# Kernel optimization log

Hardware: AMD Instinct MI355X
Metric: run time of the kernel (lower is better)

## Reference

```python
import jax, jax.numpy as jnp
import numpy as np

B, L, D, H = 2, 2048, 2048, 16
HD = D // H  # 128

def setup_inputs() -> dict:
    key = jax.random.key(0)
    ks = jax.random.split(key, 12)
    s = 1.0 / np.sqrt(D)
    inp = {
        'x': jax.random.normal(ks[0], (B, L, D), jnp.float32),
        'sin': jax.random.normal(ks[1], (L, HD // 2), jnp.float32),
        'cos': jax.random.normal(ks[2], (L, HD // 2), jnp.float32),
        'mask': jnp.tril(jnp.ones((L, L), jnp.int32))[None, None],  # causal [1,1,L,L]
        'Wq': jax.random.normal(ks[3], (D, D), jnp.float32) * s,
        'bq': jnp.zeros((D,), jnp.float32),
        'Wk': jax.random.normal(ks[4], (D, D), jnp.float32) * s,
        'bk': jnp.zeros((D,), jnp.float32),
        'Wv': jax.random.normal(ks[5], (D, D), jnp.float32) * s,
        'bv': jnp.zeros((D,), jnp.float32),
        'Wo': jax.random.normal(ks[6], (D, D), jnp.float32) * s,
        'bo': jnp.zeros((D,), jnp.float32),
    }
    return inp

def reference(x, sin, cos, mask, Wq, bq, Wk, bk, Wv, bv, Wo, bo):
    Bx, Lx, Dx = x.shape
    q = (x @ Wq.T + bq).reshape(Bx, Lx, H, HD)
    k = (x @ Wk.T + bk).reshape(Bx, Lx, H, HD)
    v = (x @ Wv.T + bv).reshape(Bx, Lx, H, HD)
    half = HD // 2
    # partial rotary: note original computes q_rot*(cos - sin) (faithful)
    rot = (cos - sin)[:, None, :]  # [L,1,half]
    q = jnp.concatenate([q[..., :half] * rot, q[..., half:]], axis=-1)
    k = jnp.concatenate([k[..., :half] * rot, k[..., half:]], axis=-1)
    q = q.transpose(0, 2, 1, 3)  # [B,H,L,hd]
    k = k.transpose(0, 2, 1, 3)
    v = v.transpose(0, 2, 1, 3)
    scores = jnp.einsum('bhqd,bhkd->bhqk', q, k) / np.sqrt(HD).astype(np.float32)
    scores = jnp.where(mask == 0, -jnp.inf, scores)
    attn = jax.nn.softmax(scores, axis=-1)
    out = jnp.einsum('bhqk,bhkd->bhqd', attn, v)
    out = out.transpose(0, 2, 1, 3).reshape(Bx, Lx, Dx)
    return out @ Wo.T + bo
```

## Files before the change

kernel.cpp:

```cpp
#include <hip/hip_runtime.h>
#include <hip/hip_bf16.h>

typedef __attribute__((ext_vector_type(8))) short short8;
typedef __attribute__((ext_vector_type(4))) ushort ushort4v;
typedef __attribute__((ext_vector_type(4))) float f32x4;

#define MFMA16(A, B, C) __builtin_amdgcn_mfma_f32_16x16x32_bf16(A, B, C, 0, 0, 0)

#define GLOAD16(gp, lp)                                        \
  __builtin_amdgcn_global_load_lds(                            \
      (__attribute__((address_space(1))) void*)(gp),           \
      (__attribute__((address_space(3))) void*)(lp), 16, 0, 0)

static constexpr int Lx = 2048, Dx = 2048, Hx = 16, HDx = 128, NBx = 2;

__device__ __forceinline__ ushort f2bu(float f) {
  __hip_bfloat16 h = __float2bfloat16(f);
  union { __hip_bfloat16 h; ushort u; } v;
  v.h = h;
  return v.u;
}

__device__ __forceinline__ short8 pack8(const float4& a, const float4& b) {
  short8 r;
  r[0] = (short)f2bu(a.x); r[1] = (short)f2bu(a.y);
  r[2] = (short)f2bu(a.z); r[3] = (short)f2bu(a.w);
  r[4] = (short)f2bu(b.x); r[5] = (short)f2bu(b.y);
  r[6] = (short)f2bu(b.z); r[7] = (short)f2bu(b.w);
  return r;
}

__global__ void convert_kernel(const float* __restrict__ x,
                               const float* __restrict__ Wq,
                               const float* __restrict__ Wk,
                               const float* __restrict__ Wv,
                               const float* __restrict__ Wo,
                               ushort* __restrict__ xb, ushort* __restrict__ wqb,
                               ushort* __restrict__ wkb, ushort* __restrict__ wvb,
                               ushort* __restrict__ wob) {
  const int y = blockIdx.y;
  const float* s;
  ushort* d;
  int n;
  switch (y) {
    case 0: s = x;  d = xb;  n = NBx * Lx * Dx; break;
    case 1: s = Wq; d = wqb; n = Dx * Dx; break;
    case 2: s = Wk; d = wkb; n = Dx * Dx; break;
    case 3: s = Wv; d = wvb; n = Dx * Dx; break;
    default: s = Wo; d = wob; n = Dx * Dx; break;
  }
  const int stride = gridDim.x * blockDim.x * 8;
  for (int i = (blockIdx.x * blockDim.x + threadIdx.x) * 8; i < n; i += stride) {
    float4 a = *(const float4*)(s + i);
    float4 b = *(const float4*)(s + i + 4);
    *(short8*)(d + i) = pack8(a, b);
  }
}

__global__ __launch_bounds__(256, 2) void qkv_kernel(
    const ushort* __restrict__ xb,
    const ushort* __restrict__ wqb, const float* __restrict__ bq,
    const ushort* __restrict__ wkb, const float* __restrict__ bk,
    const ushort* __restrict__ wvb, const float* __restrict__ bv,
    const float* __restrict__ sinT, const float* __restrict__ cosT,
    ushort* __restrict__ qw, ushort* __restrict__ kw, ushort* __restrict__ vw) {
  const int z = blockIdx.z;
  const ushort* W   = (z == 0) ? wqb : (z == 1) ? wkb : wvb;
  const float* bias = (z == 0) ? bq : (z == 1) ? bk : bv;
  ushort* outp      = (z == 0) ? qw : (z == 1) ? kw : vw;

  const int bm = blockIdx.x, bn = blockIdx.y;
  const int tid = threadIdx.x;
  const int lane = tid & 63;
  const int w = tid >> 6;
  const int l15 = tid & 15, hi = (tid >> 4) & 3;
  const int wm = (w >> 1) * 64, wn = (w & 1) * 64;

  __shared__ ushort As[2][128 * 32];
  __shared__ ushort Bs[2][128 * 32];

  const int cA = w * 2;
  const int srow = cA * 16 + (lane >> 2);
  const int scol = (lane & 3) * 8;
  const ushort* aSrc = xb + (size_t)(bm * 128 + srow) * Dx + scol;
  const ushort* bSrc = W + (size_t)(bn * 128 + srow) * Dx + scol;
  const int ldsOff = cA * 512;

#define STAGE_QKV(buf, kt)                                           \
  do {                                                               \
    const ushort* ap = aSrc + (kt) * 32;                             \
    const ushort* bp = bSrc + (kt) * 32;                             \
    GLOAD16(ap, &As[buf][ldsOff]);                                   \
    GLOAD16(ap + 16 * Dx, &As[buf][ldsOff + 512]);                   \
    GLOAD16(bp, &Bs[buf][ldsOff]);                                   \
    GLOAD16(bp + 16 * Dx, &Bs[buf][ldsOff + 512]);                   \
  } while (0)

  f32x4 acc[4][4];
#pragma unroll
  for (int i = 0; i < 4; ++i)
#pragma unroll
    for (int j = 0; j < 4; ++j) acc[i][j] = {0.f, 0.f, 0.f, 0.f};

  STAGE_QKV(0, 0);
  __syncthreads();

  int cur = 0;
  for (int kt = 0; kt < 64; ++kt) {
    if (kt < 63) STAGE_QKV(cur ^ 1, kt + 1);
    short8 af[4], bf[4];
#pragma unroll
    for (int i = 0; i < 4; ++i)
      af[i] = *(const short8*)&As[cur][(wm + i * 16 + l15) * 32 + hi * 8];
#pragma unroll
    for (int j = 0; j < 4; ++j)
      bf[j] = *(const short8*)&Bs[cur][(wn + j * 16 + l15) * 32 + hi * 8];
#pragma unroll
    for (int i = 0; i < 4; ++i)
#pragma unroll
      for (int j = 0; j < 4; ++j) acc[i][j] = MFMA16(af[i], bf[j], acc[i][j]);
    __syncthreads();
    cur ^= 1;
  }
#undef STAGE_QKV

  const float rsHD = 0.08838834764831845f;
#pragma unroll
  for (int j = 0; j < 4; ++j) {
    const int n = bn * 128 + wn + j * 16 + l15;
    const int h = n >> 7, d = n & 127;
    const float bb = bias[n];
#pragma unroll
    for (int i = 0; i < 4; ++i) {
#pragma unroll
      for (int r = 0; r < 4; ++r) {
        const int m = bm * 128 + wm + i * 16 + hi * 4 + r;
        const int b = m >> 11, l = m & (Lx - 1);
        float v = acc[i][j][r] + bb;
        if (z < 2 && d < 64) v *= (cosT[l * 64 + d] - sinT[l * 64 + d]);
        if (z == 0) v *= rsHD;
        outp[(size_t)((b * Hx + h) * Lx + l) * HDx + d] = f2bu(v);
      }
    }
  }
}

__global__ __launch_bounds__(256, 2) void attn_kernel(
    const ushort* __restrict__ qw, const ushort* __restrict__ kw,
    const ushort* __restrict__ vw, ushort* __restrict__ ctx) {
  const int qt = (int)(gridDim.x - 1) - (int)blockIdx.x;
  const int bh = blockIdx.y;
  const int b = bh >> 4, h = bh & 15;
  const int tid = threadIdx.x;
  const int w = tid >> 6, l15 = tid & 15, hi = (tid >> 4) & 3;

  const ushort* Q = qw + (size_t)bh * Lx * HDx;
  const ushort* K = kw + (size_t)bh * Lx * HDx;
  const ushort* V = vw + (size_t)bh * Lx * HDx;

  __shared__ ushort Ks[64][136];
  __shared__ ushort Vt[128][72];
  __shared__ ushort Ps[4][16][72];

  short8 qf[4];
  {
    const ushort* qr = Q + (size_t)(qt * 64 + w * 16 + l15) * HDx + hi * 8;
#pragma unroll
    for (int ds = 0; ds < 4; ++ds) qf[ds] = *(const short8*)(qr + ds * 32);
  }

  f32x4 o[8];
#pragma unroll
  for (int df = 0; df < 8; ++df) o[df] = {0.f, 0.f, 0.f, 0.f};
  float mr[4], lr[4];
#pragma unroll
  for (int r = 0; r < 4; ++r) { mr[r] = -1e30f; lr[r] = 0.f; }

  const int skrow = tid >> 2, skd = (tid & 3) * 32;
  const int svk = (tid & 15) * 4, svd = (tid >> 4) * 8;

  for (int kv = 0; kv <= qt; ++kv) {
    __syncthreads();
    {
      const ushort* kp = K + (size_t)(kv * 64 + skrow) * HDx + skd;
      short8 k0 = *(const short8*)(kp + 0), k1 = *(const short8*)(kp + 8);
      short8 k2 = *(const short8*)(kp + 16), k3 = *(const short8*)(kp + 24);
      *(short8*)&Ks[skrow][skd + 0] = k0;
      *(short8*)&Ks[skrow][skd + 8] = k1;
      *(short8*)&Ks[skrow][skd + 16] = k2;
      *(short8*)&Ks[skrow][skd + 24] = k3;
    }
    {
      const ushort* vp = V + (size_t)(kv * 64 + svk) * HDx + svd;
      short8 r0 = *(const short8*)(vp);
      short8 r1 = *(const short8*)(vp + HDx);
      short8 r2 = *(const short8*)(vp + 2 * HDx);
      short8 r3 = *(const short8*)(vp + 3 * HDx);
#pragma unroll
      for (int j = 0; j < 8; ++j) {
        ushort4v pk;
        pk[0] = (ushort)r0[j]; pk[1] = (ushort)r1[j];
        pk[2] = (ushort)r2[j]; pk[3] = (ushort)r3[j];
        *(ushort4v*)&Vt[svd + j][svk] = pk;
      }
    }
    __syncthreads();

    f32x4 s[4];
#pragma unroll
    for (int kf = 0; kf < 4; ++kf) s[kf] = {0.f, 0.f, 0.f, 0.f};
#pragma unroll
    for (int kf = 0; kf < 4; ++kf)
#pragma unroll
      for (int ds = 0; ds < 4; ++ds) {
        short8 kb = *(const short8*)&Ks[kf * 16 + l15][ds * 32 + hi * 8];
        s[kf] = MFMA16(qf[ds], kb, s[kf]);
      }

    if (kv == qt) {
#pragma unroll
      for (int kf = 0; kf < 4; ++kf)
#pragma unroll
        for (int r = 0; r < 4; ++r)
          if (kf * 16 + l15 > w * 16 + hi * 4 + r) s[kf][r] = -1e30f;
    }

    float ml[4];
#pragma unroll
    for (int r = 0; r < 4; ++r)
      ml[r] = fmaxf(fmaxf(s[0][r], s[1][r]), fmaxf(s[2][r], s[3][r]));
#pragma unroll
    for (int off = 1; off <= 8; off <<= 1)
#pragma unroll
      for (int r = 0; r < 4; ++r) ml[r] = fmaxf(ml[r], __shfl_xor(ml[r], off));
    float scl[4];
#pragma unroll
    for (int r = 0; r < 4; ++r) {
      float mn = fmaxf(mr[r], ml[r]);
      scl[r] = __expf(mr[r] - mn);
      mr[r] = mn;
    }
    float ll[4] = {0.f, 0.f, 0.f, 0.f};
#pragma unroll
    for (int kf = 0; kf < 4; ++kf)
#pragma unroll
      for (int r = 0; r < 4; ++r) {
        float p = __expf(s[kf][r] - mr[r]);
        s[kf][r] = p;
        ll[r] += p;
      }
#pragma unroll
    for (int off = 1; off <= 8; off <<= 1)
#pragma unroll
      for (int r = 0; r < 4; ++r) ll[r] += __shfl_xor(ll[r], off);
#pragma unroll
    for (int r = 0; r < 4; ++r) lr[r] = lr[r] * scl[r] + ll[r];
#pragma unroll
    for (int df = 0; df < 8; ++df)
#pragma unroll
      for (int r = 0; r < 4; ++r) o[df][r] *= scl[r];

#pragma unroll
    for (int kf = 0; kf < 4; ++kf)
#pragma unroll
      for (int r = 0; r < 4; ++r)
        Ps[w][hi * 4 + r][kf * 16 + l15] = f2bu(s[kf][r]);

    short8 pa0 = *(const short8*)&Ps[w][l15][hi * 8];
    short8 pa1 = *(const short8*)&Ps[w][l15][32 + hi * 8];
#pragma unroll
    for (int df = 0; df < 8; ++df) {
      short8 v0 = *(const short8*)&Vt[df * 16 + l15][hi * 8];
      short8 v1 = *(const short8*)&Vt[df * 16 + l15][32 + hi * 8];
      o[df] = MFMA16(pa0, v0, o[df]);
      o[df] = MFMA16(pa1, v1, o[df]);
    }
  }

  float inv[4];
#pragma unroll
  for (int r = 0; r < 4; ++r) inv[r] = 1.0f / lr[r];
  ushort* cp = ctx + (size_t)(b * Lx + qt * 64 + w * 16) * Dx + h * HDx;
#pragma unroll
  for (int df = 0; df < 8; ++df)
#pragma unroll
    for (int r = 0; r < 4; ++r)
      cp[(size_t)(hi * 4 + r) * Dx + df * 16 + l15] = f2bu(o[df][r] * inv[r]);
}

__global__ __launch_bounds__(256, 2) void oproj_kernel(
    const ushort* __restrict__ ctx, const ushort* __restrict__ wob,
    const float* __restrict__ bo, float* __restrict__ out) {
  const int bm = blockIdx.x, bn = blockIdx.y;
  const int tid = threadIdx.x;
  const int lane = tid & 63;
  const int w = tid >> 6;
  const int l15 = tid & 15, hi = (tid >> 4) & 3;
  const int wm = (w >> 1) * 64, wn = (w & 1) * 64;

  __shared__ ushort As[2][128 * 32];
  __shared__ ushort Bs[2][128 * 32];

  const int cA = w * 2;
  const int srow = cA * 16 + (lane >> 2);
  const int scol = (lane & 3) * 8;
  const ushort* aSrc = ctx + (size_t)(bm * 128 + srow) * Dx + scol;
  const ushort* bSrc = wob + (size_t)(bn * 128 + srow) * Dx + scol;
  const int ldsOff = cA * 512;

#define STAGE_O(buf, kt)                                             \
  do {                                                               \
    const ushort* ap = aSrc + (kt) * 32;                             \
    const ushort* bp = bSrc + (kt) * 32;                             \
    GLOAD16(ap, &As[buf][ldsOff]);                                   \
    GLOAD16(ap + 16 * Dx, &As[buf][ldsOff + 512]);                   \
    GLOAD16(bp, &Bs[buf][ldsOff]);                                   \
    GLOAD16(bp + 16 * Dx, &Bs[buf][ldsOff + 512]);                   \
  } while (0)

  f32x4 acc[4][4];
#pragma unroll
  for (int i = 0; i < 4; ++i)
#pragma unroll
    for (int j = 0; j < 4; ++j) acc[i][j] = {0.f, 0.f, 0.f, 0.f};

  STAGE_O(0, 0);
  __syncthreads();

  int cur = 0;
  for (int kt = 0; kt < 64; ++kt) {
    if (kt < 63) STAGE_O(cur ^ 1, kt + 1);
    short8 af[4], bf[4];
#pragma unroll
    for (int i = 0; i < 4; ++i)
      af[i] = *(const short8*)&As[cur][(wm + i * 16 + l15) * 32 + hi * 8];
#pragma unroll
    for (int j = 0; j < 4; ++j)
      bf[j] = *(const short8*)&Bs[cur][(wn + j * 16 + l15) * 32 + hi * 8];
#pragma unroll
    for (int i = 0; i < 4; ++i)
#pragma unroll
      for (int j = 0; j < 4; ++j) acc[i][j] = MFMA16(af[i], bf[j], acc[i][j]);
    __syncthreads();
    cur ^= 1;
  }
#undef STAGE_O

#pragma unroll
  for (int j = 0; j < 4; ++j) {
    const int n = bn * 128 + wn + j * 16 + l15;
    const float bb = bo[n];
#pragma unroll
    for (int i = 0; i < 4; ++i)
#pragma unroll
      for (int r = 0; r < 4; ++r) {
        const int m = bm * 128 + wm + i * 16 + hi * 4 + r;
        out[(size_t)m * Dx + n] = acc[i][j][r] + bb;
      }
  }
}

extern "C" void kernel_launch(void* const* d_in, const int* in_sizes, int n_in,
                              void* d_out, int out_size, void* d_ws, size_t ws_size,
                              hipStream_t stream) {
  (void)in_sizes; (void)n_in; (void)out_size; (void)ws_size;
  const float* x    = (const float*)d_in[0];
  const float* sinT = (const float*)d_in[1];
  const float* cosT = (const float*)d_in[2];
  const float* Wq = (const float*)d_in[4];
  const float* bq = (const float*)d_in[5];
  const float* Wk = (const float*)d_in[6];
  const float* bk = (const float*)d_in[7];
  const float* Wv = (const float*)d_in[8];
  const float* bv = (const float*)d_in[9];
  const float* Wo = (const float*)d_in[10];
  const float* bo = (const float*)d_in[11];
  float* out = (float*)d_out;

  const size_t N = (size_t)NBx * Lx * Dx;
  const size_t M = (size_t)Dx * Dx;
  ushort* qw  = (ushort*)d_ws;
  ushort* kw  = qw + N;
  ushort* vw  = kw + N;
  ushort* ctx = vw + N;
  ushort* xb  = ctx;
  ushort* wqb = ctx + N;
  ushort* wkb = wqb + M;
  ushort* wvb = wkb + M;
  ushort* wob = wvb + M;

  convert_kernel<<<dim3(1024, 5), 256, 0, stream>>>(
      x, Wq, Wk, Wv, Wo, xb, wqb, wkb, wvb, wob);
  qkv_kernel<<<dim3(32, 16, 3), 256, 0, stream>>>(
      xb, wqb, bq, wkb, bk, wvb, bv, sinT, cosT, qw, kw, vw);
  attn_kernel<<<dim3(32, 32), 256, 0, stream>>>(qw, kw, vw, ctx);
  oproj_kernel<<<dim3(32, 16), 256, 0, stream>>>(ctx, wob, bo, out);
}
```

Baseline: 545.7 us.

## Pair causal query tiles per block and register-prefetch next K/V tile

Result: faster. 456.1 us (-16.4%).

```diff
diff --git a/kernel.cpp b/kernel.cpp
--- a/kernel.cpp
+++ b/kernel.cpp
@@ -148,7 +148,7 @@
 __global__ __launch_bounds__(256, 2) void attn_kernel(
     const ushort* __restrict__ qw, const ushort* __restrict__ kw,
     const ushort* __restrict__ vw, ushort* __restrict__ ctx) {
-  const int qt = (int)(gridDim.x - 1) - (int)blockIdx.x;
+  const int pair = blockIdx.x;
   const int bh = blockIdx.y;
   const int b = bh >> 4, h = bh & 15;
   const int tid = threadIdx.x;
@@ -159,133 +159,152 @@
   const ushort* V = vw + (size_t)bh * Lx * HDx;
 
   __shared__ ushort Ks[64][136];
-  __shared__ ushort Vt[128][72];
-  __shared__ ushort Ps[4][16][72];
-
-  short8 qf[4];
-  {
-    const ushort* qr = Q + (size_t)(qt * 64 + w * 16 + l15) * HDx + hi * 8;
-#pragma unroll
-    for (int ds = 0; ds < 4; ++ds) qf[ds] = *(const short8*)(qr + ds * 32);
-  }
-
-  f32x4 o[8];
-#pragma unroll
-  for (int df = 0; df < 8; ++df) o[df] = {0.f, 0.f, 0.f, 0.f};
-  float mr[4], lr[4];
-#pragma unroll
-  for (int r = 0; r < 4; ++r) { mr[r] = -1e30f; lr[r] = 0.f; }
+  __shared__ ushort Vt[128][76];
+  __shared__ ushort Ps[4][16][76];
 
   const int skrow = tid >> 2, skd = (tid & 3) * 32;
   const int svk = (tid & 15) * 4, svd = (tid >> 4) * 8;
 
-  for (int kv = 0; kv <= qt; ++kv) {
-    __syncthreads();
+  for (int seg = 0; seg < 2; ++seg) {
+    const int qt = seg ? (31 - pair) : pair;
+
+    short8 qf[4];
     {
-      const ushort* kp = K + (size_t)(kv * 64 + skrow) * HDx + skd;
-      short8 k0 = *(const short8*)(kp + 0), k1 = *(const short8*)(kp + 8);
-      short8 k2 = *(const short8*)(kp + 16), k3 = *(const short8*)(kp + 24);
-      *(short8*)&Ks[skrow][skd + 0] = k0;
-      *(short8*)&Ks[skrow][skd + 8] = k1;
-      *(short8*)&Ks[skrow][skd + 16] = k2;
-      *(short8*)&Ks[skrow][skd + 24] = k3;
+      const ushort* qr = Q + (size_t)(qt * 64 + w * 16 + l15) * HDx + hi * 8;
+#pragma unroll
+      for (int ds = 0; ds < 4; ++ds) qf[ds] = *(const short8*)(qr + ds * 32);
     }
+
+    f32x4 o[8];
+#pragma unroll
+    for (int df = 0; df < 8; ++df) o[df] = {0.f, 0.f, 0.f, 0.f};
+    float mr[4], lr[4];
+#pragma unroll
+    for (int r = 0; r < 4; ++r) { mr[r] = -1e30f; lr[r] = 0.f; }
+
+    short8 kreg[4], vreg[4];
     {
-      const ushort* vp = V + (size_t)(kv * 64 + svk) * HDx + svd;
-      short8 r0 = *(const short8*)(vp);
-      short8 r1 = *(const short8*)(vp + HDx);
-      short8 r2 = *(const short8*)(vp + 2 * HDx);
-      short8 r3 = *(const short8*)(vp + 3 * HDx);
+      const ushort* kp = K + (size_t)skrow * HDx + skd;
+      kreg[0] = *(const short8*)(kp + 0);  kreg[1] = *(const short8*)(kp + 8);
+      kreg[2] = *(const short8*)(kp + 16); kreg[3] = *(const short8*)(kp + 24);
+      const ushort* vp = V + (size_t)svk * HDx + svd;
+      vreg[0] = *(const short8*)(vp);
+      vreg[1] = *(const short8*)(vp + HDx);
+      vreg[2] = *(const short8*)(vp + 2 * HDx);
+      vreg[3] = *(const short8*)(vp + 3 * HDx);
+    }
+
+    for (int kv = 0; kv <= qt; ++kv) {
+      __syncthreads();
+      *(short8*)&Ks[skrow][skd + 0] = kreg[0];
+      *(short8*)&Ks[skrow][skd + 8] = kreg[1];
+      *(short8*)&Ks[skrow][skd + 16] = kreg[2];
+      *(short8*)&Ks[skrow][skd + 24] = kreg[3];
 #pragma unroll
       for (int j = 0; j < 8; ++j) {
         ushort4v pk;
-        pk[0] = (ushort)r0[j]; pk[1] = (ushort)r1[j];
-        pk[2] = (ushort)r2[j]; pk[3] = (ushort)r3[j];
+        pk[0] = (ushort)vreg[0][j]; pk[1] = (ushort)vreg[1][j];
+        pk[2] = (ushort)vreg[2][j]; pk[3] = (ushort)vreg[3][j];
         *(ushort4v*)&Vt[svd + j][svk] = pk;
       }
+      __syncthreads();
+
+      if (kv < qt) {
+        const ushort* kp = K + (size_t)((kv + 1) * 64 + skrow) * HDx + skd;
+        kreg[0] = *(const short8*)(kp + 0);  kreg[1] = *(const short8*)(kp + 8);
+        kreg[2] = *(const short8*)(kp + 16); kreg[3] = *(const short8*)(kp + 24);
+        const ushort* vp = V + (size_t)((kv + 1) * 64 + svk) * HDx + svd;
+        vreg[0] = *(const short8*)(vp);
+        vreg[1] = *(const short8*)(vp + HDx);
+        vreg[2] = *(const short8*)(vp + 2 * HDx);
+        vreg[3] = *(const short8*)(vp + 3 * HDx);
+      }
+
+      f32x4 s[4];
+#pragma unroll
+      for (int kf = 0; kf < 4; ++kf) s[kf] = {0.f, 0.f, 0.f, 0.f};
+      __builtin_amdgcn_s_setprio(1);
+#pragma unroll
+      for (int kf = 0; kf < 4; ++kf)
+#pragma unroll
+        for (int ds = 0; ds < 4; ++ds) {
+          short8 kb = *(const short8*)&Ks[kf * 16 + l15][ds * 32 + hi * 8];
+          s[kf] = MFMA16(qf[ds], kb, s[kf]);
+        }
+      __builtin_amdgcn_s_setprio(0);
+
+      if (kv == qt) {
+#pragma unroll
+        for (int kf = 0; kf < 4; ++kf)
+#pragma unroll
+          for (int r = 0; r < 4; ++r)
+            if (kf * 16 + l15 > w * 16 + hi * 4 + r) s[kf][r] = -1e30f;
+      }
+
+      float ml[4];
+#pragma unroll
+      for (int r = 0; r < 4; ++r)
+        ml[r] = fmaxf(fmaxf(s[0][r], s[1][r]), fmaxf(s[2][r], s[3][r]));
+#pragma unroll
+      for (int off = 1; off <= 8; off <<= 1)
+#pragma unroll
+        for (int r = 0; r < 4; ++r) ml[r] = fmaxf(ml[r], __shfl_xor(ml[r], off));
+      float scl[4];
+#pragma unroll
+      for (int r = 0; r < 4; ++r) {
+        float mn = fmaxf(mr[r], ml[r]);
+        scl[r] = __expf(mr[r] - mn);
+        mr[r] = mn;
+      }
+      float ll[4] = {0.f, 0.f, 0.f, 0.f};
+#pragma unroll
+      for (int kf = 0; kf < 4; ++kf)
+#pragma unroll
+        for (int r = 0; r < 4; ++r) {
+          float p = __expf(s[kf][r] - mr[r]);
+          s[kf][r] = p;
+          ll[r] += p;
+        }
+#pragma unroll
+      for (int off = 1; off <= 8; off <<= 1)
+#pragma unroll
+        for (int r = 0; r < 4; ++r) ll[r] += __shfl_xor(ll[r], off);
+#pragma unroll
+      for (int r = 0; r < 4; ++r) lr[r] = lr[r] * scl[r] + ll[r];
+#pragma unroll
+      for (int df = 0; df < 8; ++df)
+#pragma unroll
+        for (int r = 0; r < 4; ++r) o[df][r] *= scl[r];
+
+#pragma unroll
+      for (int kf = 0; kf < 4; ++kf)
+#pragma unroll
+        for (int r = 0; r < 4; ++r)
+          Ps[w][hi * 4 + r][kf * 16 + l15] = f2bu(s[kf][r]);
+
+      short8 pa0 = *(const short8*)&Ps[w][l15][hi * 8];
+      short8 pa1 = *(const short8*)&Ps[w][l15][32 + hi * 8];
+      __builtin_amdgcn_s_setprio(1);
+#pragma unroll
+      for (int df = 0; df < 8; ++df) {
+        short8 v0 = *(const short8*)&Vt[df * 16 + l15][hi * 8];
+        short8 v1 = *(const short8*)&Vt[df * 16 + l15][32 + hi * 8];
+        o[df] = MFMA16(pa0, v0, o[df]);
+        o[df] = MFMA16(pa1, v1, o[df]);
+      }
+      __builtin_amdgcn_s_setprio(0);
     }
-    __syncthreads();
-
-    f32x4 s[4];
-#pragma unroll
-    for (int kf = 0; kf < 4; ++kf) s[kf] = {0.f, 0.f, 0.f, 0.f};
-#pragma unroll
-    for (int kf = 0; kf < 4; ++kf)
-#pragma unroll
-      for (int ds = 0; ds < 4; ++ds) {
-        short8 kb = *(const short8*)&Ks[kf * 16 + l15][ds * 32 + hi * 8];
-        s[kf] = MFMA16(qf[ds], kb, s[kf]);
-      }
-
-    if (kv == qt) {
-#pragma unroll
-      for (int kf = 0; kf < 4; ++kf)
-#pragma unroll
-        for (int r = 0; r < 4; ++r)
-          if (kf * 16 + l15 > w * 16 + hi * 4 + r) s[kf][r] = -1e30f;
-    }
-
-    float ml[4];
-#pragma unroll
-    for (int r = 0; r < 4; ++r)
-      ml[r] = fmaxf(fmaxf(s[0][r], s[1][r]), fmaxf(s[2][r], s[3][r]));
-#pragma unroll
-    for (int off = 1; off <= 8; off <<= 1)
-#pragma unroll
-      for (int r = 0; r < 4; ++r) ml[r] = fmaxf(ml[r], __shfl_xor(ml[r], off));
-    float scl[4];
-#pragma unroll
-    for (int r = 0; r < 4; ++r) {
-      float mn = fmaxf(mr[r], ml[r]);
-      scl[r] = __expf(mr[r] - mn);
-      mr[r] = mn;
-    }
-    float ll[4] = {0.f, 0.f, 0.f, 0.f};
-#pragma unroll
-    for (int kf = 0; kf < 4; ++kf)
-#pragma unroll
-      for (int r = 0; r < 4; ++r) {
-        float p = __expf(s[kf][r] - mr[r]);
-        s[kf][r] = p;
-        ll[r] += p;
-      }
-#pragma unroll
-    for (int off = 1; off <= 8; off <<= 1)
-#pragma unroll
-      for (int r = 0; r < 4; ++r) ll[r] += __shfl_xor(ll[r], off);
-#pragma unroll
-    for (int r = 0; r < 4; ++r) lr[r] = lr[r] * scl[r] + ll[r];
+
+    float inv[4];
+#pragma unroll
+    for (int r = 0; r < 4; ++r) inv[r] = 1.0f / lr[r];
+    ushort* cp = ctx + (size_t)(b * Lx + qt * 64 + w * 16) * Dx + h * HDx;
 #pragma unroll
     for (int df = 0; df < 8; ++df)
 #pragma unroll
-      for (int r = 0; r < 4; ++r) o[df][r] *= scl[r];
-
-#pragma unroll
-    for (int kf = 0; kf < 4; ++kf)
-#pragma unroll
       for (int r = 0; r < 4; ++r)
-        Ps[w][hi * 4 + r][kf * 16 + l15] = f2bu(s[kf][r]);
-
-    short8 pa0 = *(const short8*)&Ps[w][l15][hi * 8];
-    short8 pa1 = *(const short8*)&Ps[w][l15][32 + hi * 8];
-#pragma unroll
-    for (int df = 0; df < 8; ++df) {
-      short8 v0 = *(const short8*)&Vt[df * 16 + l15][hi * 8];
-      short8 v1 = *(const short8*)&Vt[df * 16 + l15][32 + hi * 8];
-      o[df] = MFMA16(pa0, v0, o[df]);
-      o[df] = MFMA16(pa1, v1, o[df]);
-    }
-  }
-
-  float inv[4];
-#pragma unroll
-  for (int r = 0; r < 4; ++r) inv[r] = 1.0f / lr[r];
-  ushort* cp = ctx + (size_t)(b * Lx + qt * 64 + w * 16) * Dx + h * HDx;
-#pragma unroll
-  for (int df = 0; df < 8; ++df)
-#pragma unroll
-    for (int r = 0; r < 4; ++r)
-      cp[(size_t)(hi * 4 + r) * Dx + df * 16 + l15] = f2bu(o[df][r] * inv[r]);
+        cp[(size_t)(hi * 4 + r) * Dx + df * 16 + l15] = f2bu(o[df][r] * inv[r]);
+  }
 }
 
 __global__ __launch_bounds__(256, 2) void oproj_kernel(
@@ -393,6 +412,6 @@
       x, Wq, Wk, Wv, Wo, xb, wqb, wkb, wvb, wob);
   qkv_kernel<<<dim3(32, 16, 3), 256, 0, stream>>>(
       xb, wqb, bq, wkb, bk, wvb, bv, sinT, cosT, qw, kw, vw);
-  attn_kernel<<<dim3(32, 32), 256, 0, stream>>>(qw, kw, vw, ctx);
+  attn_kernel<<<dim3(16, 32), 256, 0, stream>>>(qw, kw, vw, ctx);
   oproj_kernel<<<dim3(32, 16), 256, 0, stream>>>(ctx, wob, bo, out);
 }
```
